# Kernel optimization log

Measured on AMD Instinct MI355X. Metric: run time of the kernel, lower is better.

The kernel has to match this reference:

```python
import jax, jax.numpy as jnp
import numpy as np

B, N, BQ, BK = 2, 2048, 32, 128
NB = N // BQ
CS, CZ, CH, H, PQK, PV = 384, 128, 16, 12, 4, 8
INF, EPS = 1e5, 1e-8
CONCAT = CZ // 4 + CH + PV * 4  # per-head concat feature dim


def _ln(x, g, b):
    m = jnp.mean(x, -1, keepdims=True)
    v = jnp.mean((x - m) ** 2, -1, keepdims=True)
    return (x - m) * jax.lax.rsqrt(v + 1e-5) * g + b


def _forward(s, z, trans, rots, s_mask, key_idx,
             ln_s_g, ln_s_b, ln_z_g, ln_z_b,
             Wq, Wk, Wv, Wqp, Wkvp, Wb, Wdz, head_weights, Wout):
    sN = _ln(s, ln_s_g, ln_s_b)                     # [B,N,CS]
    zN = _ln(z, ln_z_g, ln_z_b)                     # [B,NB,BQ,BK,CZ]
    q_in = sN.reshape(B, NB, BQ, CS)                # to_queries = block reshape
    k_in = sN[:, key_idx]                           # to_keys = gather [B,NB,BK,CS]
    q_t = trans.reshape(B, NB, BQ, 3)
    q_R = rots.reshape(B, NB, BQ, 3, 3)
    k_t = trans[:, key_idx]                         # [B,NB,BK,3]
    k_R = rots[:, key_idx]                          # [B,NB,BK,3,3]

    q = (q_in @ Wq).reshape(B, NB, BQ, H, CH)
    k = (k_in @ Wk).reshape(B, NB, BK, H, CH)
    v = (k_in @ Wv).reshape(B, NB, BK, H, CH)

    # query points: local -> global frame (R p + t)
    q_pts = (q_in @ Wqp).reshape(B, NB, BQ, H * PQK, 3)
    q_pts = jnp.einsum('bnqij,bnqpj->bnqpi', q_R, q_pts) + q_t[..., None, :]
    q_pts = q_pts.reshape(B, NB, BQ, H, PQK, 3)
    kv_pts = (k_in @ Wkvp).reshape(B, NB, BK, H * (PQK + PV), 3)
    kv_pts = jnp.einsum('bnkij,bnkpj->bnkpi', k_R, kv_pts) + k_t[..., None, :]
    kv_pts = kv_pts.reshape(B, NB, BK, H, PQK + PV, 3)
    k_pts, v_pts = kv_pts[..., :PQK, :], kv_pts[..., PQK:, :]

    bbias = zN @ Wb                                 # [B,NB,BQ,BK,H]
    a = jnp.einsum('bnqhc,bnkhc->bnqkh', q, k) * np.float32(np.sqrt(1.0 / (3 * CH)))
    a = a + np.float32(np.sqrt(1.0 / 3)) * bbias

    # point-distance bias (pts_cdist=True path)
    pt = -2.0 * jnp.einsum('bnqhpd,bnkhpd->bnqkh', q_pts, k_pts)
    qn = jnp.sum(q_pts ** 2, axis=(-1, -2))         # [B,NB,BQ,H]
    kn = jnp.sum(k_pts ** 2, axis=(-1, -2))         # [B,NB,BK,H]
    pt = pt + qn[..., None, :] + kn[..., None, :, :]
    hw = jax.nn.softplus(head_weights) * np.float32(np.sqrt(1.0 / (3 * (PQK * 9.0 / 2))))
    pt = pt * hw * (-0.5)
    a = a + pt

    q_mask = s_mask.reshape(B, NB, BQ)
    k_mask = s_mask[:, key_idx]                     # [B,NB,BK]
    am = q_mask[..., :, None] * k_mask[..., None, :]  # [B,NB,BQ,BK]
    a = a + (INF * (am - 1.0))[..., None]
    a = jnp.swapaxes(a, -1, -2)                     # [B,NB,BQ,H,BK]
    a = jax.nn.softmax(a, axis=-1)

    o = jnp.einsum('bnqhk,bnkhc->bnqhc', a, v).reshape(B, NB, BQ, H * CH)
    o_pt = jnp.einsum('bnqhk,bnkhvc->bnqhvc', a, v_pts)   # [B,NB,BQ,H,PV,3]
    # invert apply: R^T (p - t), back into the query local frame
    o_pt = jnp.einsum('bnqji,bnqhvj->bnqhvi', q_R, o_pt - q_t[..., None, None, :])
    o_pt_d = jnp.sqrt(jnp.sum(o_pt ** 2, -1) + EPS).reshape(B, NB, BQ, H * PV)
    o_pt_f = o_pt.reshape(B, NB, BQ, H * PV * 3)
    pair_z = zN @ Wdz                               # [B,NB,BQ,BK,CZ//4]
    o_pair = jnp.einsum('bnqhk,bnqkc->bnqhc', a, pair_z).reshape(B, NB, BQ, H * (CZ // 4))

    feats = jnp.concatenate([o, o_pt_f, o_pt_d, o_pair], -1)  # [B,NB,BQ,H*CONCAT]
    out = feats @ Wout
    return out.reshape(B, N, CS)


def setup_inputs() -> dict:
    key = jax.random.key(0)
    ks = jax.random.split(key, 16)
    def p(i, shape, scale):
        return jax.random.normal(ks[i], shape, jnp.float32) * scale
    s = p(0, (B, N, CS), 1.0)
    z = p(1, (B, NB, BQ, BK, CZ), 1.0)
    trans = p(2, (B, N, 3), 1.0)
    rots = p(3, (B, N, 3, 3), 1.0)
    s_mask = jnp.ones((B, N), jnp.float32)
    starts = np.clip(np.arange(NB) * BQ - (BK - BQ) // 2, 0, N - BK)
    key_idx = jnp.asarray(starts[:, None] + np.arange(BK)[None, :], jnp.int32)
    return dict(
        s=s, z=z, trans=trans, rots=rots, s_mask=s_mask, key_idx=key_idx,
        ln_s_g=jnp.ones((CS,), jnp.float32), ln_s_b=jnp.zeros((CS,), jnp.float32),
        ln_z_g=jnp.ones((CZ,), jnp.float32), ln_z_b=jnp.zeros((CZ,), jnp.float32),
        Wq=p(4, (CS, H * CH), CS ** -0.5), Wk=p(5, (CS, H * CH), CS ** -0.5),
        Wv=p(6, (CS, H * CH), CS ** -0.5),
        Wqp=p(7, (CS, H * PQK * 3), CS ** -0.5),
        Wkvp=p(8, (CS, H * (PQK + PV) * 3), CS ** -0.5),
        Wb=p(9, (CZ, H), CZ ** -0.5), Wdz=p(10, (CZ, CZ // 4), CZ ** -0.5),
        head_weights=p(11, (H,), 0.5),
        Wout=p(12, (H * CONCAT, CS), 0.02),
    )


def reference(s, z, trans, rots, s_mask, key_idx,
              ln_s_g, ln_s_b, ln_z_g, ln_z_b,
              Wq, Wk, Wv, Wqp, Wkvp, Wb, Wdz, head_weights, Wout):
    return _forward(s, z, trans, rots, s_mask, key_idx,
                    ln_s_g, ln_s_b, ln_z_g, ln_z_b,
                    Wq, Wk, Wv, Wqp, Wkvp, Wb, Wdz, head_weights, Wout)
```

## Files before the change

### kernel.cpp

```cpp
#include <hip/hip_runtime.h>
#include <hip/hip_bf16.h>


typedef unsigned int uint_t;
typedef unsigned short ushort_t;
__device__ __forceinline__ float b2f(const __hip_bfloat16 x) { return __bfloat162float(x); }
__device__ __forceinline__ __hip_bfloat16 f2b(float x) { return __float2bfloat16(x); }
__device__ __forceinline__ ushort_t f2bu(float x) {
  __hip_bfloat16 h = __float2bfloat16(x);
  return *(ushort_t*)&h;
}
__device__ __forceinline__ float b2fu(ushort_t u) {
  union { uint_t i; float f; } c; c.i = ((uint_t)u) << 16; return c.f;
}
__device__ __forceinline__ uint_t pack2(float a, float b) {
  return (uint_t)f2bu(a) | ((uint_t)f2bu(b) << 16);
}
typedef __attribute__((ext_vector_type(8))) short short8x;
typedef __attribute__((ext_vector_type(4))) float floatx4;

__global__ __launch_bounds__(256) void k_ln(
    const float* __restrict__ s, const float* __restrict__ g_s,
    const float* __restrict__ b_s, float* __restrict__ sN,
    const float* __restrict__ g_z, const float* __restrict__ b_z,
    const float* __restrict__ Wb, const float* __restrict__ Wdz,
    ushort_t* __restrict__ Wt_g, float* __restrict__ uv_g,
    const float* __restrict__ Wout,
    ushort_t* __restrict__ woT_hi, ushort_t* __restrict__ woT_lo)
{
  if (blockIdx.x >= 513) {
    const int tid = threadIdx.x;
    const int c = (blockIdx.x - 513) * 4 + (tid >> 6);
    const int lane = tid & 63;
    for (int k0 = 0; k0 < 960; k0 += 64) {
      int k = k0 + lane;
      float x = Wout[(size_t)k * 384 + c];
      ushort_t hu = f2bu(x);
      woT_hi[(size_t)c * 960 + k] = hu;
      woT_lo[(size_t)c * 960 + k] = f2bu(x - b2fu(hu));
    }
    return;
  }
  if (blockIdx.x == 512) {
    const int tid = threadIdx.x;
    for (int e = tid; e < 48 * 128; e += 256) {
      int c = e >> 7, k = e & 127;
      float v = 0.f;
      if (c < 12)      v = g_z[k] * Wb[k * 12 + c];
      else if (c < 44) v = g_z[k] * Wdz[k * 32 + (c - 12)];
      Wt_g[e] = f2bu(v);
    }
    int c = tid >> 2, p = tid & 3;
    float us_ = 0.f, vs_ = 0.f;
    if (c < 44) {
      for (int k = p * 32; k < p * 32 + 32; k++) {
        float worig = (c < 12) ? Wb[k * 12 + c] : Wdz[k * 32 + (c - 12)];
        us_ += b2fu(f2bu(g_z[k] * worig));
        vs_ += b_z[k] * worig;
      }
    }
    us_ += __shfl_xor(us_, 1, 64); us_ += __shfl_xor(us_, 2, 64);
    vs_ += __shfl_xor(vs_, 1, 64); vs_ += __shfl_xor(vs_, 2, 64);
    if (p == 0 && c < 48) { uv_g[c] = us_; uv_g[48 + c] = vs_; }
    return;
  }
  const int tid = threadIdx.x;
  const int w = tid >> 6, l = tid & 63;
  #pragma unroll
  for (int ii = 0; ii < 2; ii++) {
    int row = blockIdx.x * 8 + w * 2 + ii;
    const float* sr = s + (size_t)row * 384;
    float x[6], s1 = 0.f, s2 = 0.f;
    #pragma unroll
    for (int j = 0; j < 6; j++) { x[j] = sr[l + j * 64]; s1 += x[j]; s2 += x[j] * x[j]; }
    #pragma unroll
    for (int m = 1; m < 64; m <<= 1) { s1 += __shfl_xor(s1, m, 64); s2 += __shfl_xor(s2, m, 64); }
    float mean = s1 * (1.f / 384.f);
    float var = s2 * (1.f / 384.f) - mean * mean;
    float rstd = rsqrtf(var + 1e-5f);
    float* dr = sN + (size_t)row * 384;
    #pragma unroll
    for (int j = 0; j < 6; j++) {
      int c = l + j * 64;
      dr[c] = (x[j] - mean) * rstd * g_s[c] + b_s[c];
    }
  }
}

__global__ __launch_bounds__(256) void k_zpg(
    const float* __restrict__ sN,
    const float* __restrict__ Wq, const float* __restrict__ Wk,
    const float* __restrict__ Wv, const float* __restrict__ Wqp,
    const float* __restrict__ Wkvp,
    float* __restrict__ proj,
    const float* __restrict__ z,
    const ushort_t* __restrict__ Wt_g, const float* __restrict__ uv_g,
    ushort_t* __restrict__ bbias_t, ushort_t* __restrict__ pzt)
{
  if (blockIdx.x < 1152) {
    __shared__ __align__(16) float sA[16][32];
    __shared__ __align__(16) float sB[16][128];
    const int tid = threadIdx.x;
    const int bid = blockIdx.x;
    const int mt = bid & 127;
    const int nt = bid >> 7;
    const int m0 = mt * 32, n0 = nt * 128;
    const int tm = tid >> 5, tn = tid & 31;

    const float* bsrc[2]; int bstride[2]; int bk[2];
    #pragma unroll
    for (int u = 0; u < 2; u++) {
      int idx = tid + u * 256;
      int k = idx >> 5, n4 = idx & 31;
      int col0 = n0 + n4 * 4;
      const float* p; int st;
      if (col0 < 192)      { p = Wq   + col0;         st = 192; }
      else if (col0 < 384) { p = Wk   + (col0 - 192); st = 192; }
      else if (col0 < 576) { p = Wv   + (col0 - 384); st = 192; }
      else if (col0 < 720) { p = Wqp  + (col0 - 576); st = 144; }
      else                 { p = Wkvp + (col0 - 720); st = 432; }
      bsrc[u] = p; bstride[u] = st; bk[u] = k;
    }
    const int am = tid >> 2, ak4 = tid & 3;

    float acc[4][4];
    #pragma unroll
    for (int i = 0; i < 4; i++)
      #pragma unroll
      for (int j = 0; j < 4; j++) acc[i][j] = 0.f;

    for (int k0 = 0; k0 < 384; k0 += 16) {
      #pragma unroll
      for (int u = 0; u < 2; u++) {
        float4 wv4 = *(const float4*)(bsrc[u] + (size_t)(k0 + bk[u]) * bstride[u]);
        *(float4*)&sB[bk[u]][(tid + u * 256 & 31) * 4] = wv4;
      }
      if (tid < 128) {
        float4 a4 = *(const float4*)(sN + (size_t)(m0 + am) * 384 + k0 + ak4 * 4);
        sA[ak4 * 4 + 0][am] = a4.x;
        sA[ak4 * 4 + 1][am] = a4.y;
        sA[ak4 * 4 + 2][am] = a4.z;
        sA[ak4 * 4 + 3][am] = a4.w;
      }
      __syncthreads();
      #pragma unroll
      for (int kk = 0; kk < 16; kk++) {
        float4 a4 = *(const float4*)&sA[kk][tm * 4];
        float4 b4 = *(const float4*)&sB[kk][tn * 4];
        const float* av = (const float*)&a4;
        const float* bv = (const float*)&b4;
        #pragma unroll
        for (int i = 0; i < 4; i++)
          #pragma unroll
          for (int j = 0; j < 4; j++) acc[i][j] += av[i] * bv[j];
      }
      __syncthreads();
    }
    #pragma unroll
    for (int i = 0; i < 4; i++)
      *(float4*)(proj + (size_t)(m0 + tm * 4 + i) * 1152 + n0 + tn * 4) = *(float4*)&acc[i][0];
  } else {
    const int tid = threadIdx.x;
    const int bid = blockIdx.x - 1152;
    const int w = tid >> 6, lane = tid & 63, quad = lane >> 4, r16 = lane & 15;
    const size_t row0 = (size_t)bid * 64;
    const int lrow = w * 16 + r16;
    const float* zr = z + (row0 + lrow) * 128;

    short8x bf[3][4];
    #pragma unroll
    for (int nt = 0; nt < 3; nt++)
      #pragma unroll
      for (int kk = 0; kk < 4; kk++)
        bf[nt][kk] = *(const short8x*)(Wt_g + (size_t)(nt * 16 + r16) * 128 + kk * 32 + quad * 8);

    union { short8x v; uint_t u[4]; } afu[4];
    float s1 = 0.f, s2 = 0.f;
    #pragma unroll
    for (int kk = 0; kk < 4; kk++) {
      float4 a = *(const float4*)(zr + kk * 32 + quad * 8);
      float4 b = *(const float4*)(zr + kk * 32 + quad * 8 + 4);
      s1 += a.x + a.y + a.z + a.w + b.x + b.y + b.z + b.w;
      s2 += a.x * a.x + a.y * a.y + a.z * a.z + a.w * a.w
          + b.x * b.x + b.y * b.y + b.z * b.z + b.w * b.w;
      afu[kk].u[0] = pack2(a.x, a.y);
      afu[kk].u[1] = pack2(a.z, a.w);
      afu[kk].u[2] = pack2(b.x, b.y);
      afu[kk].u[3] = pack2(b.z, b.w);
    }
    s1 += __shfl_xor(s1, 16, 64); s1 += __shfl_xor(s1, 32, 64);
    s2 += __shfl_xor(s2, 16, 64); s2 += __shfl_xor(s2, 32, 64);
    float mean = s1 * (1.f / 128.f);
    float rstd = rsqrtf(s2 * (1.f / 128.f) - mean * mean + 1e-5f);

    floatx4 acc[3] = { {0,0,0,0}, {0,0,0,0}, {0,0,0,0} };
    #pragma unroll
    for (int kk = 0; kk < 4; kk++)
      #pragma unroll
      for (int nt = 0; nt < 3; nt++)
        acc[nt] = __builtin_amdgcn_mfma_f32_16x16x32_bf16(afu[kk].v, bf[nt][kk], acc[nt], 0, 0, 0);

    float mr[4], rr[4];
    #pragma unroll
    for (int reg = 0; reg < 4; reg++) {
      int src = quad * 4 + reg;
      mr[reg] = __shfl(mean, src, 64);
      rr[reg] = __shfl(rstd, src, 64);
    }

    const int bp = bid >> 6;
    const int qk0 = (bid & 63) * 64;
    const int qloc = qk0 >> 7;
    const int kbase = (qk0 & 127) + w * 16 + quad * 4;
    #pragma unroll
    for (int nt = 0; nt < 3; nt++) {
      int c = nt * 16 + r16;
      if (c < 44) {
        float uc = uv_g[c], vc = uv_g[48 + c];
        float vals[4];
        #pragma unroll
        for (int reg = 0; reg < 4; reg++)
          vals[reg] = rr[reg] * acc[nt][reg] - mr[reg] * rr[reg] * uc + vc;
        uint2 pk = make_uint2(pack2(vals[0], vals[1]), pack2(vals[2], vals[3]));
        if (c < 12) {
          size_t el = (((size_t)(bp * 12 + c)) << 12) + qk0 + w * 16 + quad * 4;
          *(uint2*)(bbias_t + el) = pk;
        } else {
          size_t el = (((size_t)((bp * 32 + qloc) * 32 + (c - 12))) << 7) + kbase;
          *(uint2*)(pzt + el) = pk;
        }
      }
    }
  }
}

__global__ __launch_bounds__(256) void k_rot(
    const float* __restrict__ proj_g,
    const float* __restrict__ trans, const float* __restrict__ rots,
    float* __restrict__ posq, float* __restrict__ posk, float* __restrict__ posv,
    float* __restrict__ posqp, float* __restrict__ poskp, float* __restrict__ posvp,
    float* __restrict__ posqn, float* __restrict__ poskn)
{
  __shared__ __align__(16) float proj[8][1152];
  __shared__ float rt[8][12];
  const int tid = threadIdx.x;
  const int p0 = blockIdx.x * 8;

  for (int e = tid; e < 8 * 288; e += 256)
    ((float4*)&proj[0][0])[e] = ((const float4*)(proj_g + (size_t)p0 * 1152))[e];
  for (int e = tid; e < 8 * 12; e += 256) {
    int i = e / 12, c = e % 12;
    rt[i][c] = (c < 9) ? rots[(size_t)(p0 + i) * 9 + c]
                       : trans[(size_t)(p0 + i) * 3 + (c - 9)];
  }
  __syncthreads();

  for (int e = tid; e < 8 * 192; e += 256) {
    int i = e / 192, p = e % 192;
    float R0 = rt[i][0], R1 = rt[i][1], R2 = rt[i][2];
    float R3 = rt[i][3], R4 = rt[i][4], R5 = rt[i][5];
    float R6 = rt[i][6], R7 = rt[i][7], R8 = rt[i][8];
    float tx = rt[i][9], ty = rt[i][10], tz = rt[i][11];
    size_t pos = p0 + i;
    if (p < 48) {
      int base = 576 + p * 3;
      float v0 = proj[i][base], v1 = proj[i][base + 1], v2 = proj[i][base + 2];
      float o0 = R0 * v0 + R1 * v1 + R2 * v2 + tx;
      float o1 = R3 * v0 + R4 * v1 + R5 * v2 + ty;
      float o2 = R6 * v0 + R7 * v1 + R8 * v2 + tz;
      proj[i][base] = o0; proj[i][base + 1] = o1; proj[i][base + 2] = o2;
      posqp[pos * 144 + p * 3 + 0] = o0;
      posqp[pos * 144 + p * 3 + 1] = o1;
      posqp[pos * 144 + p * 3 + 2] = o2;
    } else {
      int p2 = p - 48;
      int base = 720 + p2 * 3;
      float v0 = proj[i][base], v1 = proj[i][base + 1], v2 = proj[i][base + 2];
      float o0 = R0 * v0 + R1 * v1 + R2 * v2 + tx;
      float o1 = R3 * v0 + R4 * v1 + R5 * v2 + ty;
      float o2 = R6 * v0 + R7 * v1 + R8 * v2 + tz;
      int h = p2 / 12, idx = p2 % 12;
      if (idx < 4) {
        proj[i][base] = o0; proj[i][base + 1] = o1; proj[i][base + 2] = o2;
        poskp[pos * 144 + h * 12 + idx * 3 + 0] = o0;
        poskp[pos * 144 + h * 12 + idx * 3 + 1] = o1;
        poskp[pos * 144 + h * 12 + idx * 3 + 2] = o2;
      } else {
        posvp[pos * 288 + h * 24 + (idx - 4) * 3 + 0] = o0;
        posvp[pos * 288 + h * 24 + (idx - 4) * 3 + 1] = o1;
        posvp[pos * 288 + h * 24 + (idx - 4) * 3 + 2] = o2;
      }
    }
  }
  __syncthreads();

  for (int e = tid; e < 96; e += 256) {
    int i = e / 12, h = e % 12;
    size_t pos = p0 + i;
    float qs = 0.f, ks = 0.f;
    #pragma unroll
    for (int u = 0; u < 12; u++) {
      float a_ = proj[i][576 + h * 12 + u];
      qs += a_ * a_;
      float c_ = proj[i][720 + h * 36 + u];
      ks += c_ * c_;
    }
    posqn[pos * 12 + h] = qs;
    poskn[pos * 12 + h] = ks;
  }
  for (int e = tid; e < 8 * 576; e += 256) {
    int i = e / 576, c = e % 576;
    size_t pos = p0 + i;
    float v = proj[i][c];
    if (c < 192)      posq[pos * 192 + c]         = v;
    else if (c < 384) posk[pos * 192 + (c - 192)] = v;
    else              posv[pos * 192 + (c - 384)] = v;
  }
}

__global__ __launch_bounds__(256) void k_attn(
    const float* __restrict__ posq, const float* __restrict__ posk,
    const float* __restrict__ posv, const float* __restrict__ posqp,
    const float* __restrict__ poskp, const float* __restrict__ posvp,
    const float* __restrict__ posqn, const float* __restrict__ poskn,
    const ushort_t* __restrict__ bbias_t,
    const float* __restrict__ s_mask, const int* __restrict__ key_idx,
    const float* __restrict__ trans, const float* __restrict__ rots,
    const float* __restrict__ head_w,
    float* __restrict__ feats, ushort_t* __restrict__ P_ws)
{
  __shared__ __align__(16) ushort_t sK[2 * 128 * 40];
  __shared__ __align__(16) ushort_t sV[2 * 48 * 136];
  __shared__ __align__(16) ushort_t sQ[2 * 32 * 40];
  __shared__ __align__(16) ushort_t sP[64 * 136];
  __shared__ float sOpt[64 * 25];
  __shared__ float rt[32][12];
  __shared__ float kn_l[2][128];
  __shared__ float qn_l[2][32];
  __shared__ float kmask[128];
  __shared__ float qmask[32];
  __shared__ int   kidx[128];
  __shared__ float hwe2[2];

  const int tid = threadIdx.x;
  const int bid = blockIdx.x;
  const int b = bid / 384;
  const int rem = bid % 384;
  const int nb = rem / 6;
  const int hp = rem % 6;
  const int h0 = hp * 2;
  const int rowbase = b * 2048 + nb * 32;

  if (tid < 128) kidx[tid] = key_idx[nb * 128 + tid];
  if (tid < 2) hwe2[tid] = -0.5f * 0.13608276348795434f * log1pf(expf(head_w[h0 + tid]));
  __syncthreads();

  if (tid < 128) kmask[tid] = s_mask[b * 2048 + kidx[tid]];
  if (tid < 32) qmask[tid] = s_mask[rowbase + tid];
  for (int e = tid; e < 384; e += 256) {
    int i = e / 12, c = e % 12;
    rt[i][c] = (c < 9) ? rots[(size_t)(rowbase + i) * 9 + c]
                       : trans[(size_t)(rowbase + i) * 3 + (c - 9)];
  }

  {
    int hh = tid >> 7, k = tid & 127, h = h0 + hh;
    int gk = b * 2048 + kidx[k];
    kn_l[hh][k] = poskn[(size_t)gk * 12 + h];
    float sq = 0.14433756729740643f;
    float sp = -2.f * hwe2[hh];
    const float* kr = posk + (size_t)gk * 192 + h * 16;
    #pragma unroll
    for (int c4 = 0; c4 < 4; c4++) {
      float4 v4 = *(const float4*)(kr + c4 * 4);
      uint2 pk = make_uint2(pack2(sq * v4.x, sq * v4.y), pack2(sq * v4.z, sq * v4.w));
      *(uint2*)&sK[(hh * 128 + k) * 40 + c4 * 4] = pk;
    }
    const float* kpr = poskp + (size_t)gk * 144 + h * 12;
    #pragma unroll
    for (int c4 = 0; c4 < 3; c4++) {
      float4 v4 = *(const float4*)(kpr + c4 * 4);
      uint2 pk = make_uint2(pack2(sp * v4.x, sp * v4.y), pack2(sp * v4.z, sp * v4.w));
      *(uint2*)&sK[(hh * 128 + k) * 40 + 16 + c4 * 4] = pk;
    }
    *(uint2*)&sK[(hh * 128 + k) * 40 + 28] = make_uint2(0u, 0u);
  }
  {
    int hh = tid >> 7, t7 = tid & 127, h = h0 + hh;
    int k2 = t7 >> 1, cg = t7 & 1, kk0 = k2 * 2;
    int ga = b * 2048 + kidx[kk0], gb = b * 2048 + kidx[kk0 + 1];
    if (cg == 0) {
      const float* A_ = posv + (size_t)ga * 192 + h * 16;
      const float* B_ = posv + (size_t)gb * 192 + h * 16;
      #pragma unroll
      for (int c4 = 0; c4 < 4; c4++) {
        float4 a4 = *(const float4*)(A_ + c4 * 4);
        float4 b4 = *(const float4*)(B_ + c4 * 4);
        #pragma unroll
        for (int j = 0; j < 4; j++)
          *(uint_t*)&sV[(hh * 48 + c4 * 4 + j) * 136 + kk0] =
              pack2(((const float*)&a4)[j], ((const float*)&b4)[j]);
      }
    } else {
      const float* A_ = posvp + (size_t)ga * 288 + h * 24;
      const float* B_ = posvp + (size_t)gb * 288 + h * 24;
      #pragma unroll
      for (int c4 = 0; c4 < 6; c4++) {
        float4 a4 = *(const float4*)(A_ + c4 * 4);
        float4 b4 = *(const float4*)(B_ + c4 * 4);
        #pragma unroll
        for (int j = 0; j < 4; j++)
          *(uint_t*)&sV[(hh * 48 + 16 + c4 * 4 + j) * 136 + kk0] =
              pack2(((const float*)&a4)[j], ((const float*)&b4)[j]);
      }
      #pragma unroll
      for (int j = 0; j < 8; j++)
        *(uint_t*)&sV[(hh * 48 + 40 + j) * 136 + kk0] = 0u;
    }
  }
  if (tid < 64) {
    int hh = tid >> 5, q = tid & 31, h = h0 + hh;
    qn_l[hh][q] = posqn[(size_t)(rowbase + q) * 12 + h];
    const float* qr = posq + (size_t)(rowbase + q) * 192 + h * 16;
    #pragma unroll
    for (int c4 = 0; c4 < 4; c4++) {
      float4 v4 = *(const float4*)(qr + c4 * 4);
      uint2 pk = make_uint2(pack2(v4.x, v4.y), pack2(v4.z, v4.w));
      *(uint2*)&sQ[(hh * 32 + q) * 40 + c4 * 4] = pk;
    }
    const float* qpr = posqp + (size_t)(rowbase + q) * 144 + h * 12;
    #pragma unroll
    for (int c4 = 0; c4 < 3; c4++) {
      float4 v4 = *(const float4*)(qpr + c4 * 4);
      uint2 pk = make_uint2(pack2(v4.x, v4.y), pack2(v4.z, v4.w));
      *(uint2*)&sQ[(hh * 32 + q) * 40 + 16 + c4 * 4] = pk;
    }
    *(uint2*)&sQ[(hh * 32 + q) * 40 + 28] = make_uint2(0u, 0u);
  }
  __syncthreads();

  const int w = tid >> 6, lane = tid & 63, quad = lane >> 4, r16 = lane & 15;
  const int hh = w >> 1, q0 = (w & 1) * 16;
  const int h = h0 + hh;
  const float hwe = hwe2[hh];

  short8x af = *(const short8x*)&sQ[(hh * 32 + q0 + r16) * 40 + quad * 8];
  floatx4 acc[8];
  #pragma unroll
  for (int nt = 0; nt < 8; nt++) {
    floatx4 z4 = {0.f, 0.f, 0.f, 0.f};
    short8x bf = *(const short8x*)&sK[(hh * 128 + nt * 16 + r16) * 40 + quad * 8];
    acc[nt] = __builtin_amdgcn_mfma_f32_16x16x32_bf16(af, bf, z4, 0, 0, 0);
  }

  const ushort_t* bb = bbias_t + (((size_t)((b * 64 + nb) * 12 + h)) << 12);
  float lg[8][4];
  #pragma unroll
  for (int nt = 0; nt < 8; nt++)
    #pragma unroll
    for (int reg = 0; reg < 4; reg++) {
      int qa = q0 + quad * 4 + reg;
      lg[nt][reg] = b2fu(bb[qa * 128 + nt * 16 + r16]);
    }
  float qnv[4], qmv[4];
  #pragma unroll
  for (int reg = 0; reg < 4; reg++) {
    int qa = q0 + quad * 4 + reg;
    qnv[reg] = qn_l[hh][qa]; qmv[reg] = qmask[qa];
  }
  #pragma unroll
  for (int nt = 0; nt < 8; nt++) {
    int col = nt * 16 + r16;
    float knv = kn_l[hh][col], kmv = kmask[col];
    #pragma unroll
    for (int reg = 0; reg < 4; reg++)
      lg[nt][reg] = acc[nt][reg] + 0.5773502691896258f * lg[nt][reg]
                  + hwe * (qnv[reg] + knv) + 100000.f * (qmv[reg] * kmv - 1.f);
  }
  float mx[4], sm[4];
  #pragma unroll
  for (int reg = 0; reg < 4; reg++) {
    float m = lg[0][reg];
    #pragma unroll
    for (int nt = 1; nt < 8; nt++) m = fmaxf(m, lg[nt][reg]);
    #pragma unroll
    for (int d = 1; d < 16; d <<= 1) m = fmaxf(m, __shfl_xor(m, d, 64));
    mx[reg] = m; sm[reg] = 0.f;
  }
  #pragma unroll
  for (int nt = 0; nt < 8; nt++)
    #pragma unroll
    for (int reg = 0; reg < 4; reg++) {
      float e = __expf(lg[nt][reg] - mx[reg]);
      lg[nt][reg] = e; sm[reg] += e;
    }
  #pragma unroll
  for (int reg = 0; reg < 4; reg++) {
    float s = sm[reg];
    #pragma unroll
    for (int d = 1; d < 16; d <<= 1) s += __shfl_xor(s, d, 64);
    sm[reg] = 1.f / s;
  }
  #pragma unroll
  for (int nt = 0; nt < 8; nt++)
    #pragma unroll
    for (int reg = 0; reg < 4; reg++) {
      int row = quad * 4 + reg;
      sP[(w * 16 + row) * 136 + nt * 16 + r16] = f2bu(lg[nt][reg] * sm[reg]);
    }
  short8x afp[4];
  #pragma unroll
  for (int kk = 0; kk < 4; kk++)
    afp[kk] = *(const short8x*)&sP[(w * 16 + r16) * 136 + kk * 32 + quad * 8];
  floatx4 o0 = {0.f,0.f,0.f,0.f}, o1 = {0.f,0.f,0.f,0.f}, o2 = {0.f,0.f,0.f,0.f};
  #pragma unroll
  for (int kk = 0; kk < 4; kk++) {
    short8x bv0 = *(const short8x*)&sV[(hh * 48 +  0 + r16) * 136 + kk * 32 + quad * 8];
    short8x bv1 = *(const short8x*)&sV[(hh * 48 + 16 + r16) * 136 + kk * 32 + quad * 8];
    short8x bv2 = *(const short8x*)&sV[(hh * 48 + 32 + r16) * 136 + kk * 32 + quad * 8];
    o0 = __builtin_amdgcn_mfma_f32_16x16x32_bf16(afp[kk], bv0, o0, 0, 0, 0);
    o1 = __builtin_amdgcn_mfma_f32_16x16x32_bf16(afp[kk], bv1, o1, 0, 0, 0);
    o2 = __builtin_amdgcn_mfma_f32_16x16x32_bf16(afp[kk], bv2, o2, 0, 0, 0);
  }
  #pragma unroll
  for (int reg = 0; reg < 4; reg++) {
    int qa = q0 + quad * 4 + reg;
    feats[(size_t)(rowbase + qa) * 960 + h * 16 + r16] = o0[reg];
  }
  #pragma unroll
  for (int reg = 0; reg < 4; reg++) {
    int row = quad * 4 + reg;
    sOpt[(w * 16 + row) * 25 + r16] = o1[reg];
    if (r16 < 8) sOpt[(w * 16 + row) * 25 + 16 + r16] = o2[reg];
  }
  for (int e2 = lane; e2 < 128; e2 += 64) {
    int ql = e2 >> 3, v = e2 & 7;
    int qa = q0 + ql;
    float u0 = sOpt[(w * 16 + ql) * 25 + v * 3 + 0] - rt[qa][9];
    float u1 = sOpt[(w * 16 + ql) * 25 + v * 3 + 1] - rt[qa][10];
    float u2 = sOpt[(w * 16 + ql) * 25 + v * 3 + 2] - rt[qa][11];
    float w0 = rt[qa][0] * u0 + rt[qa][3] * u1 + rt[qa][6] * u2;
    float w1 = rt[qa][1] * u0 + rt[qa][4] * u1 + rt[qa][7] * u2;
    float w2 = rt[qa][2] * u0 + rt[qa][5] * u1 + rt[qa][8] * u2;
    size_t fb = (size_t)(rowbase + qa) * 960;
    feats[fb + 192 + h * 24 + v * 3 + 0] = w0;
    feats[fb + 192 + h * 24 + v * 3 + 1] = w1;
    feats[fb + 192 + h * 24 + v * 3 + 2] = w2;
    feats[fb + 480 + h * 8 + v] = sqrtf(w0 * w0 + w1 * w1 + w2 * w2 + 1e-8f);
  }
  {
    uint_t* Pg = (uint_t*)P_ws;
    size_t pb2 = (((size_t)((b * 64 + nb) * 12 + h)) << 12) >> 1;
    #pragma unroll
    for (int ql = 0; ql < 16; ql++) {
      uint_t pv = *(const uint_t*)&sP[(w * 16 + ql) * 136 + 2 * lane];
      Pg[pb2 + (size_t)(q0 + ql) * 64 + lane] = pv;
    }
  }
}

__global__ __launch_bounds__(256) void k_opair(
    const ushort_t* __restrict__ P_ws, const ushort_t* __restrict__ pzt,
    float* __restrict__ feats)
{
  __shared__ __align__(16) ushort_t pzl[4 * 32 * 136];
  const int tid = threadIdx.x;
  const int w = tid >> 6, lane = tid & 63, quad = lane >> 4, r16 = lane & 15;
  const int bid = blockIdx.x;
  const int b = bid >> 9, rem = bid & 511, nb = rem >> 3, qg = rem & 7;
  const int q = qg * 4 + w;
  const int rowbase = b * 2048 + nb * 32;

  const uint_t* src = (const uint_t*)pzt + ((((size_t)((b * 64 + nb) * 32 + q)) << 12) >> 1);
  #pragma unroll
  for (int c = 0; c < 32; c++) {
    uint_t v = src[c * 64 + lane];
    *(uint_t*)&pzl[(w * 32 + c) * 136 + 2 * lane] = v;
  }
  const ushort_t* Pp = P_ws + ((size_t)(b * 64 + nb) * 12) * 4096
                            + (size_t)r16 * 4096 + (size_t)q * 128;
  short8x af[4];
  #pragma unroll
  for (int kk = 0; kk < 4; kk++)
    af[kk] = *(const short8x*)(Pp + kk * 32 + quad * 8);

  floatx4 acc[2] = { {0.f,0.f,0.f,0.f}, {0.f,0.f,0.f,0.f} };
  #pragma unroll
  for (int kk = 0; kk < 4; kk++) {
    #pragma unroll
    for (int nt = 0; nt < 2; nt++) {
      short8x bf = *(const short8x*)&pzl[(w * 32 + nt * 16 + r16) * 136 + kk * 32 + quad * 8];
      acc[nt] = __builtin_amdgcn_mfma_f32_16x16x32_bf16(af[kk], bf, acc[nt], 0, 0, 0);
    }
  }
  #pragma unroll
  for (int nt = 0; nt < 2; nt++)
    #pragma unroll
    for (int reg = 0; reg < 4; reg++) {
      int hrow = quad * 4 + reg;
      if (hrow < 12)
        feats[(size_t)(rowbase + q) * 960 + 576 + hrow * 32 + nt * 16 + r16] = acc[nt][reg];
    }
}

__global__ __launch_bounds__(512) void k_out(
    const float* __restrict__ feats,
    const ushort_t* __restrict__ woT_hi, const ushort_t* __restrict__ woT_lo,
    float* __restrict__ out)
{
  __shared__ __align__(16) ushort_t hiA[16 * 968];
  __shared__ __align__(16) ushort_t loA[16 * 968];
  const int tid = threadIdx.x;
  const int p0 = blockIdx.x * 16;

  for (int e = tid; e < 16 * 240; e += 512) {
    int i = e / 240, c4 = e % 240;
    float4 v = ((const float4*)&feats[(size_t)(p0 + i) * 960])[c4];
    ushort_t h0 = f2bu(v.x), h1 = f2bu(v.y), h2 = f2bu(v.z), h3 = f2bu(v.w);
    uint2 hp = make_uint2((uint_t)h0 | ((uint_t)h1 << 16), (uint_t)h2 | ((uint_t)h3 << 16));
    uint2 lp = make_uint2(pack2(v.x - b2fu(h0), v.y - b2fu(h1)),
                          pack2(v.z - b2fu(h2), v.w - b2fu(h3)));
    *(uint2*)&hiA[i * 968 + c4 * 4] = hp;
    *(uint2*)&loA[i * 968 + c4 * 4] = lp;
  }
  __syncthreads();

  const int wv = tid >> 6, lane = tid & 63, quad = lane >> 4, r16 = lane & 15;
  const int n0 = wv * 48;
  floatx4 acc[3] = { {0.f,0.f,0.f,0.f}, {0.f,0.f,0.f,0.f}, {0.f,0.f,0.f,0.f} };

  #pragma unroll 2
  for (int ks = 0; ks < 30; ks++) {
    int k0 = ks * 32;
    short8x ah = *(const short8x*)&hiA[r16 * 968 + k0 + quad * 8];
    short8x al = *(const short8x*)&loA[r16 * 968 + k0 + quad * 8];
    #pragma unroll
    for (int nt = 0; nt < 3; nt++) {
      size_t bo = (size_t)(n0 + nt * 16 + r16) * 960 + k0 + quad * 8;
      short8x bh = *(const short8x*)(woT_hi + bo);
      short8x bl = *(const short8x*)(woT_lo + bo);
      acc[nt] = __builtin_amdgcn_mfma_f32_16x16x32_bf16(ah, bh, acc[nt], 0, 0, 0);
      acc[nt] = __builtin_amdgcn_mfma_f32_16x16x32_bf16(al, bh, acc[nt], 0, 0, 0);
      acc[nt] = __builtin_amdgcn_mfma_f32_16x16x32_bf16(ah, bl, acc[nt], 0, 0, 0);
    }
  }
  #pragma unroll
  for (int nt = 0; nt < 3; nt++)
    #pragma unroll
    for (int reg = 0; reg < 4; reg++) {
      int row = quad * 4 + reg;
      out[(size_t)(p0 + row) * 384 + n0 + nt * 16 + r16] = acc[nt][reg];
    }
}

extern "C" void kernel_launch(void* const* d_in, const int* in_sizes, int n_in,
                              void* d_out, int out_size, void* d_ws, size_t ws_size,
                              hipStream_t stream) {
  const float* s      = (const float*)d_in[0];
  const float* z      = (const float*)d_in[1];
  const float* trans  = (const float*)d_in[2];
  const float* rots   = (const float*)d_in[3];
  const float* s_mask = (const float*)d_in[4];
  const int*   key_idx= (const int*)d_in[5];
  const float* ln_s_g = (const float*)d_in[6];
  const float* ln_s_b = (const float*)d_in[7];
  const float* ln_z_g = (const float*)d_in[8];
  const float* ln_z_b = (const float*)d_in[9];
  const float* Wq     = (const float*)d_in[10];
  const float* Wk     = (const float*)d_in[11];
  const float* Wv     = (const float*)d_in[12];
  const float* Wqp    = (const float*)d_in[13];
  const float* Wkvp   = (const float*)d_in[14];
  const float* Wb     = (const float*)d_in[15];
  const float* Wdz    = (const float*)d_in[16];
  const float* head_w = (const float*)d_in[17];
  const float* Wout   = (const float*)d_in[18];

  char* wsb = (char*)d_ws;
  float* posq  = (float*)(wsb + 0);
  float* posk  = (float*)(wsb + 3145728);
  float* posv  = (float*)(wsb + 6291456);
  float* posqp = (float*)(wsb + 9437184);
  float* poskp = (float*)(wsb + 11796480);
  float* posvp = (float*)(wsb + 14155776);
  float* posqn = (float*)(wsb + 18874368);
  float* poskn = (float*)(wsb + 19070976);
  float* feats = (float*)(wsb + 19267584);
  float* sN    = (float*)(wsb + 19267584);
  float* proj  = (float*)(wsb + 34996224);
  ushort_t* bbias_t = (ushort_t*)(wsb + 53870592);
  ushort_t* pzt     = (ushort_t*)(wsb + 66453504);
  ushort_t* P_ws    = (ushort_t*)(wsb + 100007936);
  ushort_t* Wt_ws   = (ushort_t*)(wsb + 112590848);
  float*    uv_ws   = (float*)(wsb + 112603136);
  ushort_t* woT_hi  = (ushort_t*)(wsb + 112603520);
  ushort_t* woT_lo  = (ushort_t*)(wsb + 113340800);

  k_ln<<<609, 256, 0, stream>>>(s, ln_s_g, ln_s_b, sN,
                                ln_z_g, ln_z_b, Wb, Wdz, Wt_ws, uv_ws,
                                Wout, woT_hi, woT_lo);
  k_zpg<<<9344, 256, 0, stream>>>(sN, Wq, Wk, Wv, Wqp, Wkvp, proj,
                                  z, Wt_ws, uv_ws, bbias_t, pzt);
  k_rot<<<512, 256, 0, stream>>>(proj, trans, rots,
                                 posq, posk, posv, posqp, poskp, posvp, posqn, poskn);
  k_attn<<<768, 256, 0, stream>>>(posq, posk, posv, posqp, poskp, posvp, posqn, poskn,
                                  bbias_t, s_mask, key_idx, trans, rots, head_w,
                                  feats, P_ws);
  k_opair<<<1024, 256, 0, stream>>>(P_ws, pzt, feats);
  k_out<<<256, 512, 0, stream>>>(feats, woT_hi, woT_lo, (float*)d_out);
}
```

Measured before the change: 562.9 us.

## Compute QKV/point projection with split-bf16 MFMA instead of fp32 SIMT GEMM

The fused projection GEMM (4096x1152x384) moves from a shared-memory fp32 FMA tile loop to bf16 MFMA 16x16x32 instructions. Precision is kept by splitting each operand into hi and lo bf16 parts and using three MFMAs per tile. The concatenated weights are pre-transposed and split into hi/lo bf16 arrays by extra blocks in k_ln, and the projection block count shrinks from 1152 to 256. Weight B operands are read directly from global memory without LDS staging, which may make the kernel memory-latency bound.

```diff
diff --git a/kernel.cpp b/kernel.cpp
--- a/kernel.cpp
+++ b/kernel.cpp
@@ -26,8 +26,30 @@
     const float* __restrict__ Wb, const float* __restrict__ Wdz,
     ushort_t* __restrict__ Wt_g, float* __restrict__ uv_g,
     const float* __restrict__ Wout,
-    ushort_t* __restrict__ woT_hi, ushort_t* __restrict__ woT_lo)
+    ushort_t* __restrict__ woT_hi, ushort_t* __restrict__ woT_lo,
+    const float* __restrict__ Wq, const float* __restrict__ Wk,
+    const float* __restrict__ Wv, const float* __restrict__ Wqp,
+    const float* __restrict__ Wkvp,
+    ushort_t* __restrict__ wcT_hi, ushort_t* __restrict__ wcT_lo)
 {
+  if (blockIdx.x >= 609) {
+    const int tid = threadIdx.x;
+    const int c = (blockIdx.x - 609) * 4 + (tid >> 6);
+    const int lane = tid & 63;
+    for (int k0 = 0; k0 < 384; k0 += 64) {
+      int k = k0 + lane;
+      float x;
+      if (c < 192)      x = Wq[(size_t)k * 192 + c];
+      else if (c < 384) x = Wk[(size_t)k * 192 + (c - 192)];
+      else if (c < 576) x = Wv[(size_t)k * 192 + (c - 384)];
+      else if (c < 720) x = Wqp[(size_t)k * 144 + (c - 576)];
+      else              x = Wkvp[(size_t)k * 432 + (c - 720)];
+      ushort_t hu = f2bu(x);
+      wcT_hi[(size_t)c * 384 + k] = hu;
+      wcT_lo[(size_t)c * 384 + k] = f2bu(x - b2fu(hu));
+    }
+    return;
+  }
   if (blockIdx.x >= 513) {
     const int tid = threadIdx.x;
     const int c = (blockIdx.x - 513) * 4 + (tid >> 6);
@@ -89,80 +111,60 @@
 
 __global__ __launch_bounds__(256) void k_zpg(
     const float* __restrict__ sN,
-    const float* __restrict__ Wq, const float* __restrict__ Wk,
-    const float* __restrict__ Wv, const float* __restrict__ Wqp,
-    const float* __restrict__ Wkvp,
+    const ushort_t* __restrict__ wcT_hi, const ushort_t* __restrict__ wcT_lo,
     float* __restrict__ proj,
     const float* __restrict__ z,
     const ushort_t* __restrict__ Wt_g, const float* __restrict__ uv_g,
     ushort_t* __restrict__ bbias_t, ushort_t* __restrict__ pzt)
 {
-  if (blockIdx.x < 1152) {
-    __shared__ __align__(16) float sA[16][32];
-    __shared__ __align__(16) float sB[16][128];
-    const int tid = threadIdx.x;
-    const int bid = blockIdx.x;
-    const int mt = bid & 127;
-    const int nt = bid >> 7;
-    const int m0 = mt * 32, n0 = nt * 128;
-    const int tm = tid >> 5, tn = tid & 31;
-
-    const float* bsrc[2]; int bstride[2]; int bk[2];
-    #pragma unroll
-    for (int u = 0; u < 2; u++) {
-      int idx = tid + u * 256;
-      int k = idx >> 5, n4 = idx & 31;
-      int col0 = n0 + n4 * 4;
-      const float* p; int st;
-      if (col0 < 192)      { p = Wq   + col0;         st = 192; }
-      else if (col0 < 384) { p = Wk   + (col0 - 192); st = 192; }
-      else if (col0 < 576) { p = Wv   + (col0 - 384); st = 192; }
-      else if (col0 < 720) { p = Wqp  + (col0 - 576); st = 144; }
-      else                 { p = Wkvp + (col0 - 720); st = 432; }
-      bsrc[u] = p; bstride[u] = st; bk[u] = k;
-    }
-    const int am = tid >> 2, ak4 = tid & 3;
-
-    float acc[4][4];
-    #pragma unroll
-    for (int i = 0; i < 4; i++)
+  const int tid = threadIdx.x;
+  const int w = tid >> 6, lane = tid & 63, quad = lane >> 4, r16 = lane & 15;
+
+  if (blockIdx.x < 256) {
+    __shared__ __align__(16) ushort_t hiA[16 * 392];
+    __shared__ __align__(16) ushort_t loA[16 * 392];
+    const int p0 = blockIdx.x * 16;
+
+    for (int e = tid; e < 16 * 96; e += 256) {
+      int i = e / 96, c4 = e % 96;
+      float4 v = *(const float4*)(sN + (size_t)(p0 + i) * 384 + c4 * 4);
+      ushort_t h0 = f2bu(v.x), h1 = f2bu(v.y), h2 = f2bu(v.z), h3 = f2bu(v.w);
+      uint2 hp = make_uint2((uint_t)h0 | ((uint_t)h1 << 16), (uint_t)h2 | ((uint_t)h3 << 16));
+      uint2 lp = make_uint2(pack2(v.x - b2fu(h0), v.y - b2fu(h1)),
+                            pack2(v.z - b2fu(h2), v.w - b2fu(h3)));
+      *(uint2*)&hiA[i * 392 + c4 * 4] = hp;
+      *(uint2*)&loA[i * 392 + c4 * 4] = lp;
+    }
+    __syncthreads();
+
+    #pragma unroll
+    for (int half = 0; half < 2; half++) {
+      const int n0 = w * 288 + half * 144;
+      floatx4 acc[9];
       #pragma unroll
-      for (int j = 0; j < 4; j++) acc[i][j] = 0.f;
-
-    for (int k0 = 0; k0 < 384; k0 += 16) {
+      for (int nt = 0; nt < 9; nt++) acc[nt] = (floatx4){0.f, 0.f, 0.f, 0.f};
+
+      for (int ks = 0; ks < 12; ks++) {
+        short8x ah = *(const short8x*)&hiA[r16 * 392 + ks * 32 + quad * 8];
+        short8x al = *(const short8x*)&loA[r16 * 392 + ks * 32 + quad * 8];
+        #pragma unroll
+        for (int nt = 0; nt < 9; nt++) {
+          size_t bo = (size_t)(n0 + nt * 16 + r16) * 384 + ks * 32 + quad * 8;
+          short8x bh = *(const short8x*)(wcT_hi + bo);
+          short8x bl = *(const short8x*)(wcT_lo + bo);
+          acc[nt] = __builtin_amdgcn_mfma_f32_16x16x32_bf16(ah, bh, acc[nt], 0, 0, 0);
+          acc[nt] = __builtin_amdgcn_mfma_f32_16x16x32_bf16(al, bh, acc[nt], 0, 0, 0);
+          acc[nt] = __builtin_amdgcn_mfma_f32_16x16x32_bf16(ah, bl, acc[nt], 0, 0, 0);
+        }
+      }
       #pragma unroll
-      for (int u = 0; u < 2; u++) {
-        float4 wv4 = *(const float4*)(bsrc[u] + (size_t)(k0 + bk[u]) * bstride[u]);
-        *(float4*)&sB[bk[u]][(tid + u * 256 & 31) * 4] = wv4;
-      }
-      if (tid < 128) {
-        float4 a4 = *(const float4*)(sN + (size_t)(m0 + am) * 384 + k0 + ak4 * 4);
-        sA[ak4 * 4 + 0][am] = a4.x;
-        sA[ak4 * 4 + 1][am] = a4.y;
-        sA[ak4 * 4 + 2][am] = a4.z;
-        sA[ak4 * 4 + 3][am] = a4.w;
-      }
-      __syncthreads();
-      #pragma unroll
-      for (int kk = 0; kk < 16; kk++) {
-        float4 a4 = *(const float4*)&sA[kk][tm * 4];
-        float4 b4 = *(const float4*)&sB[kk][tn * 4];
-        const float* av = (const float*)&a4;
-        const float* bv = (const float*)&b4;
+      for (int nt = 0; nt < 9; nt++)
         #pragma unroll
-        for (int i = 0; i < 4; i++)
-          #pragma unroll
-          for (int j = 0; j < 4; j++) acc[i][j] += av[i] * bv[j];
-      }
-      __syncthreads();
-    }
-    #pragma unroll
-    for (int i = 0; i < 4; i++)
-      *(float4*)(proj + (size_t)(m0 + tm * 4 + i) * 1152 + n0 + tn * 4) = *(float4*)&acc[i][0];
+        for (int reg = 0; reg < 4; reg++)
+          proj[(size_t)(p0 + quad * 4 + reg) * 1152 + n0 + nt * 16 + r16] = acc[nt][reg];
+    }
   } else {
-    const int tid = threadIdx.x;
-    const int bid = blockIdx.x - 1152;
-    const int w = tid >> 6, lane = tid & 63, quad = lane >> 4, r16 = lane & 15;
+    const int bid = blockIdx.x - 256;
     const size_t row0 = (size_t)bid * 64;
     const int lrow = w * 16 + r16;
     const float* zr = z + (row0 + lrow) * 128;
@@ -695,11 +697,14 @@
   float*    uv_ws   = (float*)(wsb + 112603136);
   ushort_t* woT_hi  = (ushort_t*)(wsb + 112603520);
   ushort_t* woT_lo  = (ushort_t*)(wsb + 113340800);
-
-  k_ln<<<609, 256, 0, stream>>>(s, ln_s_g, ln_s_b, sN,
+  ushort_t* wcT_hi  = (ushort_t*)(wsb + 114078080);
+  ushort_t* wcT_lo  = (ushort_t*)(wsb + 114962816);
+
+  k_ln<<<897, 256, 0, stream>>>(s, ln_s_g, ln_s_b, sN,
                                 ln_z_g, ln_z_b, Wb, Wdz, Wt_ws, uv_ws,
-                                Wout, woT_hi, woT_lo);
-  k_zpg<<<9344, 256, 0, stream>>>(sN, Wq, Wk, Wv, Wqp, Wkvp, proj,
+                                Wout, woT_hi, woT_lo,
+                                Wq, Wk, Wv, Wqp, Wkvp, wcT_hi, wcT_lo);
+  k_zpg<<<8448, 256, 0, stream>>>(sN, wcT_hi, wcT_lo, proj,
                                   z, Wt_ws, uv_ws, bbias_t, pzt);
   k_rot<<<512, 256, 0, stream>>>(proj, trans, rots,
                                  posq, posk, posv, posqp, poskp, posvp, posqn, poskn);
```

Result: slower. 577.0 us (+2.5%).
